# Kernel tuning notes

Measured on AMD Instinct MI355X. Metric: run time of the kernel, lower is better.

## Reference

```python
import jax, jax.numpy as jnp
import numpy as np
import math

B, S, D, H = 1, 2048, 2048, 16
DH = D // H  # 128
HALF = DH // 2  # 64


def setup_inputs() -> dict:
    key = jax.random.key(0)
    ks = jax.random.split(key, 6)
    x = jax.random.normal(ks[0], (B, S, D), dtype=jnp.float32)
    # rotary frequencies: freqs_cis = exp(i * t * theta), theta_j = 10000^{-2j/DH}
    inv_freq = 1.0 / (10000.0 ** (np.arange(0, DH, 2, dtype=np.float32) / DH))  # [HALF]
    t = np.arange(S, dtype=np.float32)
    angles = np.outer(t, inv_freq)  # [S, HALF]
    freqs_cos = jnp.asarray(np.cos(angles), dtype=jnp.float32)
    freqs_sin = jnp.asarray(np.sin(angles), dtype=jnp.float32)
    # additive causal mask [1,1,S,S]
    mask = jnp.triu(jnp.full((S, S), -1e9, dtype=jnp.float32), k=1)[None, None]
    scale = 0.02
    wq = jax.random.normal(ks[1], (D, D), dtype=jnp.float32) * scale
    wk = jax.random.normal(ks[2], (D, D), dtype=jnp.float32) * scale
    wv = jax.random.normal(ks[3], (D, D), dtype=jnp.float32) * scale
    wo = jax.random.normal(ks[4], (D, D), dtype=jnp.float32) * scale
    return {"x": x, "freqs_cos": freqs_cos, "freqs_sin": freqs_sin, "mask": mask,
            "wq": wq, "wk": wk, "wv": wv, "wo": wo, "start_pos": 0}


def _apply_rope(t, cos, sin):
    # t: [B,S,H,DH]; cos/sin: [S,HALF] broadcast as [1,S,1,HALF]
    tr = t.reshape(*t.shape[:-1], HALF, 2)
    even, odd = tr[..., 0], tr[..., 1]
    c = cos[None, :, None, :]
    s = sin[None, :, None, :]
    out_even = even * c - odd * s
    out_odd = even * s + odd * c
    return jnp.stack([out_even, out_odd], axis=-1).reshape(t.shape)


def reference(x, freqs_cos, freqs_sin, mask, wq, wk, wv, wo, start_pos):
    bsz, seqlen, _ = x.shape
    q = (x @ wq.T).reshape(bsz, seqlen, H, DH)
    k = (x @ wk.T).reshape(bsz, seqlen, H, DH)
    v = (x @ wv.T).reshape(bsz, seqlen, H, DH)
    q = _apply_rope(q, freqs_cos, freqs_sin)
    k = _apply_rope(k, freqs_cos, freqs_sin)
    q = q.transpose(0, 2, 1, 3)  # [B,H,S,DH]
    k = k.transpose(0, 2, 1, 3)
    v = v.transpose(0, 2, 1, 3)
    scores = jnp.einsum('bhqd,bhkd->bhqk', q, k) / math.sqrt(DH) + mask
    probs = jax.nn.softmax(scores, axis=-1)
    out = jnp.einsum('bhqk,bhkd->bhqd', probs, v)  # [B,H,S,DH]
    # faithful to original: transpose(2,3) then view(bsz, seqlen, dim)
    out = out.transpose(0, 1, 3, 2).reshape(bsz, seqlen, D)
    return out @ wo.T
```

## Files before the change

### kernel.cpp

```cpp
#include <hip/hip_runtime.h>

typedef unsigned short u16;
typedef unsigned int   u32;
typedef short  short8   __attribute__((ext_vector_type(8)));
typedef float  floatx4  __attribute__((ext_vector_type(4)));
typedef u16    ushortx2 __attribute__((ext_vector_type(2)));
typedef u16    ushortx4 __attribute__((ext_vector_type(4)));

__device__ __forceinline__ float bf2f(u16 u) {
  union { u32 i; float f; } v; v.i = ((u32)u) << 16; return v.f;
}
__device__ __forceinline__ u16 f2bf(float x) {
  union { float f; u32 i; } v; v.f = x;
  u32 r = v.i + 0x7FFFu + ((v.i >> 16) & 1u);
  return (u16)(r >> 16);
}

#if __has_builtin(__builtin_amdgcn_exp2f)
#define EXP2F(x) __builtin_amdgcn_exp2f(x)
#else
#define EXP2F(x) __exp2f(x)
#endif

#define GLOAD_LDS16(gptr, lptr)                                                   \
  __builtin_amdgcn_global_load_lds(                                               \
      (const __attribute__((address_space(1))) void*)(gptr),                      \
      (__attribute__((address_space(3))) void*)(lptr), 16, 0, 0)

#define WAITV(n) asm volatile("s_waitcnt vmcnt(" #n ")" ::: "memory")
#define WAITL    asm volatile("s_waitcnt lgkmcnt(0)" ::: "memory")
#define BAR      __builtin_amdgcn_s_barrier()

__global__ __launch_bounds__(256) void cvt_all(
    const floatx4* __restrict__ x,  const floatx4* __restrict__ wq,
    const floatx4* __restrict__ wk, const floatx4* __restrict__ wv,
    const floatx4* __restrict__ wo,
    ushortx4* __restrict__ xb, ushortx4* __restrict__ wqkv,
    ushortx4* __restrict__ wob) {
  int i = blockIdx.x * 256 + threadIdx.x;
  const floatx4* in; ushortx4* out;
  switch (blockIdx.y) {
    case 0:  in = x;  out = xb; break;
    case 1:  in = wq; out = wqkv; break;
    case 2:  in = wk; out = wqkv + (size_t)1048576; break;
    case 3:  in = wv; out = wqkv + (size_t)2097152; break;
    default: in = wo; out = wob; break;
  }
  floatx4 v = in[i];
  ushortx4 o;
  o.x = f2bf(v.x); o.y = f2bf(v.y); o.z = f2bf(v.z); o.w = f2bf(v.w);
  out[i] = o;
}

__global__ __launch_bounds__(512, 2) void gemm256_bt(
    const u16* __restrict__ A, const u16* __restrict__ B, u16* __restrict__ C,
    int N, int K, int lda, int ldb, int ldc) {
  const int cpx = gridDim.x >> 3;
  const int wg = ((int)blockIdx.x & 7) * cpx + ((int)blockIdx.x >> 3);
  const int ntn = N / 192;
  const int m0 = (wg / ntn) << 8;
  const int n0 = (wg % ntn) * 192;

  __shared__ __align__(16) u16 As[2][256][64];
  __shared__ __align__(16) u16 Bs[2][192][64];

  const int t = threadIdx.x;
  const int lane = t & 63;
  const int wave = t >> 6;
  const int wr = wave >> 2;
  const int wc = wave & 3;
  const int quad = lane >> 4;
  const int mrow = lane & 15;
  const int sw = mrow & 7;

  const int srow = lane >> 3;
  const int gso  = ((lane & 7) ^ srow) << 3;

  const u16* gA = A + (size_t)(m0 + (wave << 3) + srow) * lda + gso;
  const u16* gB = B + (size_t)(n0 + (wave << 3) + srow) * ldb + gso;

  floatx4 acc[8][3] = {};
  short8 afr[4][2], bfr[3][2];

  const int NT = K >> 6;

#define ST_A(nb, h, kt)                                                        \
  do {                                                                         \
    GLOAD_LDS16(gA + (size_t)((h) * 128) * lda + ((kt) << 6),                  \
                &As[nb][(h) * 128 + (wave << 3)][0]);                          \
    GLOAD_LDS16(gA + (size_t)((h) * 128 + 64) * lda + ((kt) << 6),             \
                &As[nb][(h) * 128 + 64 + (wave << 3)][0]);                     \
  } while (0)
#define ST_B1(nb, c, kt)                                                       \
  do {                                                                         \
    GLOAD_LDS16(gB + (size_t)((c) * 64) * ldb + ((kt) << 6),                   \
                &Bs[nb][(c) * 64 + (wave << 3)][0]);                           \
  } while (0)

#define LDA4(bf, base_row)                                                     \
  do {                                                                         \
    _Pragma("unroll") for (int i_ = 0; i_ < 4; i_++)                           \
      _Pragma("unroll") for (int kk_ = 0; kk_ < 2; kk_++)                      \
        afr[i_][kk_] = *(const short8*)&As[bf][(base_row) + (i_ << 4) + mrow]  \
                            [(((kk_ << 2) | quad) ^ sw) << 3];                 \
  } while (0)
#define LDB1(bf, j)                                                            \
  do {                                                                         \
    _Pragma("unroll") for (int kk_ = 0; kk_ < 2; kk_++)                        \
      bfr[j][kk_] = *(const short8*)&Bs[bf][(j) * 64 + (wc << 4) + mrow]       \
          [(((kk_ << 2) | quad) ^ sw) << 3];                                   \
  } while (0)
#define MMQ8(ilo, j)                                                           \
  do {                                                                         \
    __builtin_amdgcn_s_setprio(1);                                             \
    _Pragma("unroll") for (int kk_ = 0; kk_ < 2; kk_++)                        \
      _Pragma("unroll") for (int i_ = 0; i_ < 4; i_++)                         \
        acc[(ilo) + i_][j] = __builtin_amdgcn_mfma_f32_16x16x32_bf16(          \
            afr[i_][kk_], bfr[j][kk_], acc[(ilo) + i_][j], 0, 0, 0);           \
    __builtin_amdgcn_s_setprio(0);                                             \
  } while (0)

  ST_A(0, 0, 0); ST_B1(0, 0, 0); ST_B1(0, 1, 0); ST_B1(0, 2, 0); ST_A(0, 1, 0);
  WAITV(3);
  BAR;

  for (int kt = 0; kt < NT - 1; kt++) {
    const int bf = kt & 1, nb = bf ^ 1;
    LDA4(bf, (wr << 6));
    LDB1(bf, 0);
    LDB1(bf, 1);
    ST_A(nb, 0, kt + 1);
    ST_B1(nb, 0, kt + 1);
    WAITV(3);
    BAR;
    MMQ8(0, 0);
    MMQ8(0, 1);
    LDB1(bf, 2);
    ST_B1(nb, 1, kt + 1);
    ST_B1(nb, 2, kt + 1);
    BAR;
    MMQ8(0, 2);
    LDA4(bf, 128 + (wr << 6));
    MMQ8(4, 0);
    ST_A(nb, 1, kt + 1);
    WAITV(3);
    BAR;
    MMQ8(4, 1);
    MMQ8(4, 2);
  }
  {
    const int bf = (NT - 1) & 1;
    LDA4(bf, (wr << 6));
    LDB1(bf, 0);
    LDB1(bf, 1);
    WAITV(0);
    BAR;
    MMQ8(0, 0);
    MMQ8(0, 1);
    LDB1(bf, 2);
    BAR;
    MMQ8(0, 2);
    LDA4(bf, 128 + (wr << 6));
    MMQ8(4, 0);
    BAR;
    MMQ8(4, 1);
    MMQ8(4, 2);
  }

#pragma unroll
  for (int i = 0; i < 8; i++) {
    int row0 = m0 + ((i >= 4) ? 128 : 0) + (wr << 6) + ((i & 3) << 4) + (quad << 2);
#pragma unroll
    for (int j = 0; j < 3; j++) {
      int col = n0 + j * 64 + (wc << 4) + mrow;
#pragma unroll
      for (int r = 0; r < 4; r++)
        C[(size_t)(row0 + r) * ldc + col] = f2bf(acc[i][j][r]);
    }
  }
#undef ST_A
#undef ST_B1
#undef LDA4
#undef LDB1
#undef MMQ8
}

__global__ __launch_bounds__(256) void gemm_bt(
    const u16* __restrict__ A, const u16* __restrict__ B, void* __restrict__ Cv,
    int M, int N, int K, int lda, int ldb, int ldc,
    long batchA, long batchB, long batchC, int outBF16) {
  const int m0 = blockIdx.y << 7;
  const int n0 = blockIdx.x << 7;

  A += (long)blockIdx.z * batchA;
  B += (long)blockIdx.z * batchB;
  const long cbase = (long)blockIdx.z * batchC;

  __shared__ __align__(16) u16 As[128][64];
  __shared__ __align__(16) u16 Bs[128][64];

  const int t = threadIdx.x;
  const int lane = t & 63;
  const int wave = t >> 6;
  const int wm = (wave >> 1) << 6;
  const int wn = (wave & 1) << 6;
  const int quad = lane >> 4;
  const int mrow = lane & 15;
  const int sw8 = mrow & 7;

  floatx4 acc[4][4] = {};

  const int srow = lane >> 3;
  const int gseg = (((lane & 7) ^ srow) << 3);
  const u16* gA = A + (long)(m0 + (wave << 5) + srow) * lda + gseg;
  const u16* gB = B + (long)(n0 + (wave << 5) + srow) * ldb + gseg;

  for (int k0 = 0; k0 < K; k0 += 64) {
    __syncthreads();
#pragma unroll
    for (int ii = 0; ii < 4; ii++) {
      GLOAD_LDS16(gA + k0 + (size_t)(ii << 3) * lda, &As[(wave << 5) + (ii << 3)][0]);
      GLOAD_LDS16(gB + k0 + (size_t)(ii << 3) * ldb, &Bs[(wave << 5) + (ii << 3)][0]);
    }
    __syncthreads();

#pragma unroll
    for (int kh = 0; kh < 2; kh++) {
      const int sidx = ((kh << 2) | quad) ^ sw8;
      short8 af[4], bfr[4];
#pragma unroll
      for (int i = 0; i < 4; i++)
        af[i] = *(const short8*)&As[wm + (i << 4) + mrow][sidx << 3];
#pragma unroll
      for (int j = 0; j < 4; j++)
        bfr[j] = *(const short8*)&Bs[wn + (j << 4) + mrow][sidx << 3];
#pragma unroll
      for (int i = 0; i < 4; i++)
#pragma unroll
        for (int j = 0; j < 4; j++)
          acc[i][j] = __builtin_amdgcn_mfma_f32_16x16x32_bf16(af[i], bfr[j], acc[i][j], 0, 0, 0);
    }
  }

#pragma unroll
  for (int i = 0; i < 4; i++) {
    int row0 = m0 + wm + (i << 4) + (quad << 2);
#pragma unroll
    for (int j = 0; j < 4; j++) {
      int col = n0 + wn + (j << 4) + mrow;
#pragma unroll
      for (int r = 0; r < 4; r++) {
        long idx = cbase + (long)(row0 + r) * ldc + col;
        float val = acc[i][j][r];
        if (outBF16) ((u16*)Cv)[idx] = f2bf(val);
        else         ((float*)Cv)[idx] = val;
      }
    }
  }
}

__global__ __launch_bounds__(256) void transpose_v(const u16* __restrict__ src,
                                                   u16* __restrict__ dst) {
  __shared__ u16 tile[64][68];
  const int d0 = blockIdx.x << 6;
  const int s0 = blockIdx.y << 6;
  const int tx = (threadIdx.x & 15) << 2;
  const int ty = threadIdx.x >> 4;
#pragma unroll
  for (int rr = 0; rr < 64; rr += 16) {
    ushortx4 v = *(const ushortx4*)(src + (size_t)(s0 + ty + rr) * 6144 + d0 + tx);
    *(ushortx4*)&tile[ty + rr][tx] = v;
  }
  __syncthreads();
#pragma unroll
  for (int rr = 0; rr < 64; rr += 16) {
    int r = ty + rr;
    ushortx4 o;
    o.x = tile[tx + 0][r]; o.y = tile[tx + 1][r];
    o.z = tile[tx + 2][r]; o.w = tile[tx + 3][r];
    *(ushortx4*)(dst + (size_t)(d0 + r) * 2048 + s0 + tx) = o;
  }
}

__global__ __launch_bounds__(256) void rope_qk(u16* __restrict__ qkv,
                                               const float* __restrict__ cs,
                                               const float* __restrict__ sn) {
  int idx = blockIdx.x * 256 + threadIdx.x;
  int p = idx & 63;
  int h = (idx >> 6) & 15;
  int s = idx >> 10;
  float c  = cs[(s << 6) | p];
  float si = sn[(s << 6) | p];
  float scale = blockIdx.y ? 1.0f : 0.12751743f;
  size_t off = (size_t)s * 6144 + (blockIdx.y ? 2048 : 0) + (h << 7) + (p << 1);
  ushortx2 eo = *(ushortx2*)(qkv + off);
  float e = bf2f(eo.x), o = bf2f(eo.y);
  ushortx2 r;
  r.x = f2bf((e * c - o * si) * scale);
  r.y = f2bf((e * si + o * c) * scale);
  *(ushortx2*)(qkv + off) = r;
}

__global__ __launch_bounds__(256, 2) void flash_attn(
    const u16* __restrict__ QKVp, const u16* __restrict__ VTp,
    u16* __restrict__ ATp) {
  const int r0id = (int)blockIdx.x + ((int)blockIdx.y << 5);
  const int h    = r0id & 15;
  const int qsub = 31 - (r0id >> 4);
  const int q0 = qsub << 6;
  const int ktmax = qsub >> 1;

  __shared__ __align__(16) u16 Ks[128][128];
  __shared__ __align__(16) u16 Vs[128][128];
  __shared__ __align__(16) u16 Ps[64][128];

  const int t = threadIdx.x;
  const int lane = t & 63;
  const int wave = t >> 6;
  const int quad = lane >> 4;
  const int mrow = lane & 15;
  const int sw   = mrow & 7;
  const int wmS = (wave & 1) << 5;
  const int wnS = (wave >> 1) << 6;
  const int wmV = (wave >> 1) << 6;
  const int wnP = (wave & 1) << 5;

  const int r4  = lane >> 4;
  const int seg = lane & 15;
  const int c0 = ((seg ^ r4) << 3);
  const int c4 = ((seg ^ (r4 + 4)) << 3);

  const u16* qbase = QKVp + (size_t)q0 * 6144 + (h << 7);
  const u16* kbase = QKVp + 2048 + (h << 7);
  const u16* vbase = VTp + (size_t)(h << 7) * 2048;

  short8 aq[2][4];
#pragma unroll
  for (int i = 0; i < 2; i++)
#pragma unroll
    for (int kk = 0; kk < 4; kk++)
      aq[i][kk] = *(const short8*)(qbase + (size_t)(wmS + (i << 4) + mrow) * 6144 +
                                   (kk << 5) + (quad << 3));

  const short8 ones = {0x3F80, 0x3F80, 0x3F80, 0x3F80,
                       0x3F80, 0x3F80, 0x3F80, 0x3F80};

  floatx4 Oa[4][2] = {};
  floatx4 Oa1[2] = {};

  const float C2 = 23.083120654223414f;

  for (int kt = 0; kt <= ktmax; kt++) {
    __syncthreads();
    {
      int rr0 = wave << 5;
#pragma unroll
      for (int ii = 0; ii < 8; ii++) {
        int rr = rr0 + (ii << 2);
        GLOAD_LDS16(kbase + (size_t)((kt << 7) + rr + r4) * 6144 + ((ii & 1) ? c4 : c0),
                    &Ks[rr][0]);
        GLOAD_LDS16(vbase + (size_t)(rr + r4) * 2048 + (kt << 7) + ((ii & 1) ? c4 : c0),
                    &Vs[rr][0]);
      }
    }
    __syncthreads();

    floatx4 sa[2][4] = {};
#pragma unroll
    for (int kk = 0; kk < 4; kk++) {
      short8 bk[4];
#pragma unroll
      for (int j = 0; j < 4; j++)
        bk[j] = *(const short8*)&Ks[wnS + (j << 4) + mrow][(((kk << 2) | quad) ^ sw) << 3];
#pragma unroll
      for (int i = 0; i < 2; i++)
#pragma unroll
        for (int j = 0; j < 4; j++)
          sa[i][j] = __builtin_amdgcn_mfma_f32_16x16x32_bf16(aq[i][kk], bk[j], sa[i][j], 0, 0, 0);
    }
    if (kt == ktmax) {
#pragma unroll
      for (int i = 0; i < 2; i++)
#pragma unroll
        for (int j = 0; j < 4; j++)
#pragma unroll
          for (int r = 0; r < 4; r++) {
            int ql = q0 + wmS + (i << 4) + (quad << 2) + r;
            int sl = (kt << 7) + wnS + (j << 4) + mrow;
            if (sl > ql) sa[i][j][r] = -1e30f;
          }
    }
#pragma unroll
    for (int i = 0; i < 2; i++)
#pragma unroll
      for (int j = 0; j < 4; j++)
#pragma unroll
        for (int r = 0; r < 4; r++) {
          int row = wmS + (i << 4) + (quad << 2) + r;
          int col = wnS + (j << 4) + mrow;
          Ps[row][((((col >> 3) ^ (row & 7)) << 3) | (col & 7))] =
              f2bf(EXP2F(sa[i][j][r] - C2));
        }
    __syncthreads();

#pragma unroll
    for (int kk = 0; kk < 4; kk++) {
      short8 av[4], bp[2];
#pragma unroll
      for (int i = 0; i < 4; i++)
        av[i] = *(const short8*)&Vs[wmV + (i << 4) + mrow][(((kk << 2) | quad) ^ sw) << 3];
#pragma unroll
      for (int j = 0; j < 2; j++)
        bp[j] = *(const short8*)&Ps[wnP + (j << 4) + mrow][(((kk << 2) | quad) ^ sw) << 3];
#pragma unroll
      for (int i = 0; i < 4; i++)
#pragma unroll
        for (int j = 0; j < 2; j++)
          Oa[i][j] = __builtin_amdgcn_mfma_f32_16x16x32_bf16(av[i], bp[j], Oa[i][j], 0, 0, 0);
#pragma unroll
      for (int j = 0; j < 2; j++)
        Oa1[j] = __builtin_amdgcn_mfma_f32_16x16x32_bf16(ones, bp[j], Oa1[j], 0, 0, 0);
    }
  }

  float linv[2];
#pragma unroll
  for (int j = 0; j < 2; j++) linv[j] = 1.f / Oa1[j][0];
#pragma unroll
  for (int i = 0; i < 4; i++) {
    int drow = (h << 7) + wmV + (i << 4) + (quad << 2);
#pragma unroll
    for (int j = 0; j < 2; j++) {
      int col = q0 + wnP + (j << 4) + mrow;
#pragma unroll
      for (int r = 0; r < 4; r++)
        ATp[(size_t)(drow + r) * 2048 + col] = f2bf(Oa[i][j][r] * linv[j]);
    }
  }
}

__global__ __launch_bounds__(256) void reduce2(const floatx4* __restrict__ a,
                                               const floatx4* __restrict__ b,
                                               floatx4* __restrict__ o) {
  int i = blockIdx.x * 256 + threadIdx.x;
  o[i] = a[i] + b[i];
}

extern "C" void kernel_launch(void* const* d_in, const int* in_sizes, int n_in,
                              void* d_out, int out_size, void* d_ws, size_t ws_size,
                              hipStream_t stream) {
  const float* x  = (const float*)d_in[0];
  const float* fc = (const float*)d_in[1];
  const float* fs = (const float*)d_in[2];
  const float* wq = (const float*)d_in[4];
  const float* wk = (const float*)d_in[5];
  const float* wv = (const float*)d_in[6];
  const float* wo = (const float*)d_in[7];
  float* out = (float*)d_out;

  char* ws = (char*)d_ws;
  const size_t MB = 1024 * 1024;
  u16*   XB   = (u16*)(ws + 0 * MB);
  u16*   WQKV = (u16*)(ws + 8 * MB);
  u16*   WOb  = (u16*)(ws + 32 * MB);
  u16*   QKV  = (u16*)(ws + 40 * MB);
  u16*   VT   = (u16*)(ws + 64 * MB);
  u16*   AT   = (u16*)(ws + 72 * MB);
  float* PART = (float*)(ws + 80 * MB);

  int use_split = (ws_size >= 113 * MB);

  dim3 blk(256);
  cvt_all<<<dim3(4096, 5), blk, 0, stream>>>(
      (const floatx4*)x, (const floatx4*)wq, (const floatx4*)wk,
      (const floatx4*)wv, (const floatx4*)wo,
      (ushortx4*)XB, (ushortx4*)WQKV, (ushortx4*)WOb);

  gemm256_bt<<<dim3(256), dim3(512), 0, stream>>>(XB, WQKV, QKV,
                                                  6144, 2048, 2048, 2048, 6144);

  transpose_v<<<dim3(32, 32), blk, 0, stream>>>(QKV + 4096, VT);
  rope_qk<<<dim3(8192, 2), blk, 0, stream>>>(QKV, fc, fs);

  flash_attn<<<dim3(32, 16), blk, 0, stream>>>(QKV, VT, AT);

  if (use_split) {
    gemm_bt<<<dim3(16, 16, 2), blk, 0, stream>>>(AT, WOb, PART, 2048, 2048, 1024,
                                                 2048, 2048, 2048,
                                                 1024, 1024, (long)2048 * 2048, 0);
    reduce2<<<4096, blk, 0, stream>>>((const floatx4*)PART,
                                      (const floatx4*)(PART + (size_t)2048 * 2048),
                                      (floatx4*)out);
  } else {
    gemm_bt<<<dim3(16, 16, 1), blk, 0, stream>>>(AT, WOb, out, 2048, 2048, 2048,
                                                 2048, 2048, 2048, 0, 0, 0, 0);
  }
}
```

Measured before the change: 274.6 us.

## Prefetch next K tile during PV and split K/V staging with fine-grained waits

Reorganizes the attention loop so the next K tile is loaded into LDS while the current P·V MFMAs run, and V for the next tile is loaded after PV completes. The full-block syncthreads pairs are replaced with explicit vmcnt/lgkmcnt waits and barriers. It also raises wave priority around MFMA bursts via s_setprio. The aim is to hide global-to-LDS latency behind compute. The cost is extra barriers per iteration, and the V load is still exposed because only K overlaps with compute.

```diff
diff --git a/kernel.cpp b/kernel.cpp
--- a/kernel.cpp
+++ b/kernel.cpp
@@ -334,6 +334,27 @@
   const u16* kbase = QKVp + 2048 + (h << 7);
   const u16* vbase = VTp + (size_t)(h << 7) * 2048;
 
+#define STAGE_K(kt)                                                            \
+  do {                                                                         \
+    int rr0_ = wave << 5;                                                      \
+    _Pragma("unroll") for (int ii_ = 0; ii_ < 8; ii_++) {                      \
+      int rr_ = rr0_ + (ii_ << 2);                                             \
+      GLOAD_LDS16(kbase + (size_t)(((kt) << 7) + rr_ + r4) * 6144 +            \
+                      ((ii_ & 1) ? c4 : c0),                                   \
+                  &Ks[rr_][0]);                                                \
+    }                                                                          \
+  } while (0)
+#define STAGE_V(kt)                                                            \
+  do {                                                                         \
+    int rr0_ = wave << 5;                                                      \
+    _Pragma("unroll") for (int ii_ = 0; ii_ < 8; ii_++) {                      \
+      int rr_ = rr0_ + (ii_ << 2);                                             \
+      GLOAD_LDS16(vbase + (size_t)(rr_ + r4) * 2048 + ((kt) << 7) +            \
+                      ((ii_ & 1) ? c4 : c0),                                   \
+                  &Vs[rr_][0]);                                                \
+    }                                                                          \
+  } while (0)
+
   short8 aq[2][4];
 #pragma unroll
   for (int i = 0; i < 2; i++)
@@ -350,21 +371,12 @@
 
   const float C2 = 23.083120654223414f;
 
+  STAGE_K(0);
+  STAGE_V(0);
+  WAITV(8);
+  BAR;
+
   for (int kt = 0; kt <= ktmax; kt++) {
-    __syncthreads();
-    {
-      int rr0 = wave << 5;
-#pragma unroll
-      for (int ii = 0; ii < 8; ii++) {
-        int rr = rr0 + (ii << 2);
-        GLOAD_LDS16(kbase + (size_t)((kt << 7) + rr + r4) * 6144 + ((ii & 1) ? c4 : c0),
-                    &Ks[rr][0]);
-        GLOAD_LDS16(vbase + (size_t)(rr + r4) * 2048 + (kt << 7) + ((ii & 1) ? c4 : c0),
-                    &Vs[rr][0]);
-      }
-    }
-    __syncthreads();
-
     floatx4 sa[2][4] = {};
 #pragma unroll
     for (int kk = 0; kk < 4; kk++) {
@@ -372,11 +384,13 @@
 #pragma unroll
       for (int j = 0; j < 4; j++)
         bk[j] = *(const short8*)&Ks[wnS + (j << 4) + mrow][(((kk << 2) | quad) ^ sw) << 3];
+      __builtin_amdgcn_s_setprio(1);
 #pragma unroll
       for (int i = 0; i < 2; i++)
 #pragma unroll
         for (int j = 0; j < 4; j++)
           sa[i][j] = __builtin_amdgcn_mfma_f32_16x16x32_bf16(aq[i][kk], bk[j], sa[i][j], 0, 0, 0);
+      __builtin_amdgcn_s_setprio(0);
     }
     if (kt == ktmax) {
 #pragma unroll
@@ -401,7 +415,11 @@
           Ps[row][((((col >> 3) ^ (row & 7)) << 3) | (col & 7))] =
               f2bf(EXP2F(sa[i][j][r] - C2));
         }
-    __syncthreads();
+    WAITV(0);
+    WAITL;
+    BAR;
+
+    if (kt < ktmax) STAGE_K(kt + 1);
 
 #pragma unroll
     for (int kk = 0; kk < 4; kk++) {
@@ -412,6 +430,7 @@
 #pragma unroll
       for (int j = 0; j < 2; j++)
         bp[j] = *(const short8*)&Ps[wnP + (j << 4) + mrow][(((kk << 2) | quad) ^ sw) << 3];
+      __builtin_amdgcn_s_setprio(1);
 #pragma unroll
       for (int i = 0; i < 4; i++)
 #pragma unroll
@@ -420,8 +439,17 @@
 #pragma unroll
       for (int j = 0; j < 2; j++)
         Oa1[j] = __builtin_amdgcn_mfma_f32_16x16x32_bf16(ones, bp[j], Oa1[j], 0, 0, 0);
-    }
-  }
+      __builtin_amdgcn_s_setprio(0);
+    }
+    WAITL;
+    BAR;
+
+    if (kt < ktmax) STAGE_V(kt + 1);
+    WAITV(8);
+    BAR;
+  }
+#undef STAGE_K
+#undef STAGE_V
 
   float linv[2];
 #pragma unroll
```

After: 275.9 us. No clear change (+0.5%).
